# Kernel optimization log

Hardware: AMD Instinct MI355X
Metric: run time of the kernel (lower is better)

Reference implementation:

```python
import jax, jax.numpy as jnp
import numpy as np

MB, NUM, LENTH, SIZE, OUT = 16, 128, 64, 256, 256
DIN = (LENTH + 1) * 2  # aux_lenth = 0


def setup_inputs() -> dict:
    key = jax.random.key(0)
    ks = jax.random.split(key, 9)
    s = 0.05
    return {
        "in_": jax.random.normal(ks[0], (MB, NUM, LENTH), dtype=jnp.float32),
        "W1": jax.random.normal(ks[1], (DIN, SIZE), dtype=jnp.float32) * s,
        "b1": jax.random.normal(ks[2], (SIZE,), dtype=jnp.float32) * s,
        "W2": jax.random.normal(ks[3], (SIZE, SIZE), dtype=jnp.float32) * s,
        "b2": jax.random.normal(ks[4], (SIZE,), dtype=jnp.float32) * s,
        "W3": jax.random.normal(ks[5], (SIZE, SIZE), dtype=jnp.float32) * s,
        "b3": jax.random.normal(ks[6], (SIZE,), dtype=jnp.float32) * s,
        "W4": jax.random.normal(ks[7], (SIZE, OUT), dtype=jnp.float32) * s,
        "b4": jax.random.normal(ks[8], (OUT,), dtype=jnp.float32) * s,
    }


def reference(in_, W1, b1, W2, b2, W3, b3, W4, b4):
    mb, num, _ = in_.shape
    # append coordinate channel: coord[i] = i  -> [mb, num, lenth+1]
    coord = jnp.broadcast_to(
        jnp.arange(num, dtype=in_.dtype)[None, :, None], (mb, num, 1)
    )
    x = jnp.concatenate([in_, coord], axis=2)  # [mb, num, L1], L1 = lenth+1
    L1 = x.shape[2]
    # pairwise: x_full[b, a, j] = concat(x[b, j], x[b, a])
    x_i = jnp.broadcast_to(x[:, None, :, :], (mb, num, num, L1))  # varies over j
    x_j = jnp.broadcast_to(x[:, :, None, :], (mb, num, num, L1))  # varies over a
    x_full = jnp.concatenate([x_i, x_j], axis=3)  # [mb, num, num, 2*L1]
    h = x_full.reshape(mb * num * num, 2 * L1)
    h = jax.nn.relu(h @ W1 + b1)
    h = jax.nn.relu(h @ W2 + b2)
    h = jax.nn.relu(h @ W3 + b3)
    h = jax.nn.relu(h @ W4 + b4)  # [mb*num*num, OUT]
    x_g = h.reshape(mb, num * num, -1).sum(axis=1)  # [mb, OUT]
    return x_g
```

## Files before the change

kernel.cpp:

```cpp
#include <hip/hip_runtime.h>
#include <hip/hip_bf16.h>

using short8 = __attribute__((ext_vector_type(8))) short;
using f32x4  = __attribute__((ext_vector_type(4))) float;

#define MBATCH 16
#define NUMV   128
#define LEN    64
#define SZ     256

__device__ __forceinline__ unsigned short bfbits(float x) {
  union { float f; unsigned u; } c; c.f = x;
  return (unsigned short)((c.u + 0x8000u) >> 16);
}

__global__ void uv_prep(const float* __restrict__ in_, const float* __restrict__ W1,
                        const float* __restrict__ b1,
                        float* __restrict__ u, float* __restrict__ v) {
  int bn = blockIdx.x;
  int n  = bn & (NUMV - 1);
  int s  = threadIdx.x;
  __shared__ float xs[LEN];
  if (s < LEN) xs[s] = in_[bn * LEN + s];
  __syncthreads();
  float fn = (float)n;
  float uu = fn * W1[64 * SZ + s];
  float vv = fn * W1[129 * SZ + s] + b1[s];
  for (int c = 0; c < LEN; ++c) {
    uu = fmaf(xs[c], W1[c * SZ + s], uu);
    vv = fmaf(xs[c], W1[(65 + c) * SZ + s], vv);
  }
  u[bn * SZ + s] = uu;
  v[bn * SZ + s] = vv;
}

__global__ void w_prep(const float* __restrict__ W2, const float* __restrict__ W3,
                       const float* __restrict__ W4, short* __restrict__ wlay) {
  int L = blockIdx.x >> 3, kb = blockIdx.x & 7;
  const float* W = (L == 0) ? W2 : (L == 1) ? W3 : W4;
  int m = threadIdx.x >> 6, lane = threadIdx.x & 63;
  int l16 = lane & 15, q = lane >> 4;
  for (int wv = 0; wv < 4; ++wv) {
    int ch = wv * 64 + m * 16 + l16;
    short8 pk;
    for (int i = 0; i < 8; ++i)
      pk[i] = (short)bfbits(W[(kb * 32 + q * 8 + i) * SZ + ch]);
    int f = ((L * 8 + kb) * 4 + wv) * 4 + m;
    reinterpret_cast<short8*>(wlay)[f * 64 + lane] = pk;
  }
}

__global__ __launch_bounds__(256, 4) void fused_mlp(
    const float* __restrict__ u, const float* __restrict__ v,
    const short* __restrict__ wlay,
    const float* __restrict__ b2, const float* __restrict__ b3, const float* __restrict__ b4,
    float* __restrict__ partial) {
  __shared__ __align__(16) short hbuf[64 * 256];

  int wg = blockIdx.x;
  int b = wg >> 8, a = (wg >> 1) & 127, jh = wg & 1;
  int tid = threadIdx.x;
  int wave = tid >> 6, lane = tid & 63;
  int l16 = lane & 15, q = lane >> 4;

  const char* wptr = (const char*)wlay + wave * 4096 + lane * 16;

  short8 aw[4];
  #pragma unroll
  for (int m = 0; m < 4; ++m)
    aw[m] = *reinterpret_cast<const short8*>(wptr + m * 1024);

  {
    const float4* ub = (const float4*)(u + (size_t)b * NUMV * SZ) + jh * 64 * 64;
    const float4* vb = (const float4*)(v + ((size_t)b * NUMV + a) * SZ);
    #pragma unroll
    for (int it = 0; it < 16; ++it) {
      int flat = tid + it * 256;
      int jr = flat >> 6, c4 = flat & 63;
      float4 uu = ub[jr * 64 + c4];
      float4 vv = vb[c4];
      unsigned lo = (unsigned)bfbits(fmaxf(uu.x + vv.x, 0.f))
                  | ((unsigned)bfbits(fmaxf(uu.y + vv.y, 0.f)) << 16);
      unsigned hi = (unsigned)bfbits(fmaxf(uu.z + vv.z, 0.f))
                  | ((unsigned)bfbits(fmaxf(uu.w + vv.w, 0.f)) << 16);
      int byte = (jr * 512 + c4 * 8) ^ ((jr & 7) << 4);
      uint2 pk; pk.x = lo; pk.y = hi;
      *reinterpret_cast<uint2*>((char*)hbuf + byte) = pk;
    }
  }

  __syncthreads();

  #pragma unroll
  for (int L = 0; L < 3; ++L) {
    const float* bb = (L == 0) ? b2 : (L == 1) ? b3 : b4;

    f32x4 acc[4][4];
    #pragma unroll
    for (int m = 0; m < 4; ++m)
      #pragma unroll
      for (int n = 0; n < 4; ++n)
        acc[m][n] = f32x4{0.f, 0.f, 0.f, 0.f};

    #pragma unroll
    for (int kb = 0; kb < 8; ++kb) {
      bool more = (L * 8 + kb < 23);
      short8 bfr0, bfr1;
      {
        int row0 = 0 * 16 + l16, row1 = 1 * 16 + l16;
        bfr0 = *reinterpret_cast<const short8*>((char*)hbuf +
               ((row0 * 512 + kb * 64 + q * 16) ^ ((row0 & 7) << 4)));
        bfr1 = *reinterpret_cast<const short8*>((char*)hbuf +
               ((row1 * 512 + kb * 64 + q * 16) ^ ((row1 & 7) << 4)));
      }
      #pragma unroll
      for (int m = 0; m < 4; ++m) {
        acc[m][0] = __builtin_amdgcn_mfma_f32_16x16x32_bf16(aw[m], bfr0, acc[m][0], 0, 0, 0);
        acc[m][1] = __builtin_amdgcn_mfma_f32_16x16x32_bf16(aw[m], bfr1, acc[m][1], 0, 0, 0);
      }
      short8 bfr2, bfr3;
      {
        int row2 = 2 * 16 + l16, row3 = 3 * 16 + l16;
        bfr2 = *reinterpret_cast<const short8*>((char*)hbuf +
               ((row2 * 512 + kb * 64 + q * 16) ^ ((row2 & 7) << 4)));
        bfr3 = *reinterpret_cast<const short8*>((char*)hbuf +
               ((row3 * 512 + kb * 64 + q * 16) ^ ((row3 & 7) << 4)));
      }
      #pragma unroll
      for (int m = 0; m < 4; ++m) {
        acc[m][2] = __builtin_amdgcn_mfma_f32_16x16x32_bf16(aw[m], bfr2, acc[m][2], 0, 0, 0);
        acc[m][3] = __builtin_amdgcn_mfma_f32_16x16x32_bf16(aw[m], bfr3, acc[m][3], 0, 0, 0);
        if (more)
          aw[m] = *reinterpret_cast<const short8*>(wptr + 16384 + m * 1024);
      }
      wptr += 16384;
    }

    __syncthreads();

    if (L < 2) {
      #pragma unroll
      for (int m = 0; m < 4; ++m) {
        f32x4 bv = *reinterpret_cast<const f32x4*>(bb + wave * 64 + m * 16 + q * 4);
        int ch = wave * 64 + m * 16 + q * 4;
        #pragma unroll
        for (int n = 0; n < 4; ++n) {
          int row = n * 16 + l16;
          f32x4 t = acc[m][n];
          unsigned lo = (unsigned)bfbits(fmaxf(t[0] + bv[0], 0.f))
                      | ((unsigned)bfbits(fmaxf(t[1] + bv[1], 0.f)) << 16);
          unsigned hi = (unsigned)bfbits(fmaxf(t[2] + bv[2], 0.f))
                      | ((unsigned)bfbits(fmaxf(t[3] + bv[3], 0.f)) << 16);
          int byte = (row * 512 + ch * 2) ^ ((row & 7) << 4);
          uint2 pk; pk.x = lo; pk.y = hi;
          *reinterpret_cast<uint2*>((char*)hbuf + byte) = pk;
        }
      }
      __syncthreads();
    } else {
      #pragma unroll
      for (int m = 0; m < 4; ++m) {
        f32x4 bv = *reinterpret_cast<const f32x4*>(bb + wave * 64 + m * 16 + q * 4);
        f32x4 s = f32x4{0.f, 0.f, 0.f, 0.f};
        #pragma unroll
        for (int n = 0; n < 4; ++n) {
          s[0] += fmaxf(acc[m][n][0] + bv[0], 0.f);
          s[1] += fmaxf(acc[m][n][1] + bv[1], 0.f);
          s[2] += fmaxf(acc[m][n][2] + bv[2], 0.f);
          s[3] += fmaxf(acc[m][n][3] + bv[3], 0.f);
        }
        #pragma unroll
        for (int r = 0; r < 4; ++r) {
          float x = s[r];
          x += __shfl_xor(x, 1);
          x += __shfl_xor(x, 2);
          x += __shfl_xor(x, 4);
          x += __shfl_xor(x, 8);
          s[r] = x;
        }
        if (l16 == 0) {
          float4 o; o.x = s[0]; o.y = s[1]; o.z = s[2]; o.w = s[3];
          *reinterpret_cast<float4*>(partial + (size_t)wg * SZ + wave * 64 + m * 16 + q * 4) = o;
        }
      }
    }
  }
}

__global__ void reduce_partials(const float* __restrict__ partial, float* __restrict__ out) {
  int b = blockIdx.x;
  int s = threadIdx.x;
  const float* p = partial + (size_t)b * 256 * SZ + s;
  float acc = 0.f;
  for (int i = 0; i < 256; ++i) acc += p[(size_t)i * SZ];
  out[b * SZ + s] = acc;
}

extern "C" void kernel_launch(void* const* d_in, const int* in_sizes, int n_in,
                              void* d_out, int out_size, void* d_ws, size_t ws_size,
                              hipStream_t stream) {
  const float* in_ = (const float*)d_in[0];
  const float* W1  = (const float*)d_in[1];
  const float* b1  = (const float*)d_in[2];
  const float* W2  = (const float*)d_in[3];
  const float* b2  = (const float*)d_in[4];
  const float* W3  = (const float*)d_in[5];
  const float* b3  = (const float*)d_in[6];
  const float* W4  = (const float*)d_in[7];
  const float* b4  = (const float*)d_in[8];
  float* out = (float*)d_out;

  char* ws = (char*)d_ws;
  float* u       = (float*)(ws);
  float* v       = (float*)(ws + (2u << 20));
  short* wlay    = (short*)(ws + (4u << 20));
  float* partial = (float*)(ws + (4u << 20) + (1u << 19));

  uv_prep<<<MBATCH * NUMV, 256, 0, stream>>>(in_, W1, b1, u, v);
  w_prep<<<24, 256, 0, stream>>>(W2, W3, W4, wlay);
  fused_mlp<<<MBATCH * NUMV * 2, 256, 0, stream>>>(u, v, wlay, b2, b3, b4, partial);
  reduce_partials<<<MBATCH, 256, 0, stream>>>(partial, out);
}
```

Baseline: 150.2 us.

## Split fused MLP rows across eight waves per workgroup

```diff
diff --git a/kernel.cpp b/kernel.cpp
--- a/kernel.cpp
+++ b/kernel.cpp
@@ -50,7 +50,7 @@
   }
 }
 
-__global__ __launch_bounds__(256, 4) void fused_mlp(
+__global__ __launch_bounds__(512, 4) void fused_mlp(
     const float* __restrict__ u, const float* __restrict__ v,
     const short* __restrict__ wlay,
     const float* __restrict__ b2, const float* __restrict__ b3, const float* __restrict__ b4,
@@ -61,9 +61,10 @@
   int b = wg >> 8, a = (wg >> 1) & 127, jh = wg & 1;
   int tid = threadIdx.x;
   int wave = tid >> 6, lane = tid & 63;
+  int wch = wave & 3, wrow = wave >> 2;
   int l16 = lane & 15, q = lane >> 4;
 
-  const char* wptr = (const char*)wlay + wave * 4096 + lane * 16;
+  const char* wptr = (const char*)wlay + wch * 4096 + lane * 16;
 
   short8 aw[4];
   #pragma unroll
@@ -74,8 +75,8 @@
     const float4* ub = (const float4*)(u + (size_t)b * NUMV * SZ) + jh * 64 * 64;
     const float4* vb = (const float4*)(v + ((size_t)b * NUMV + a) * SZ);
     #pragma unroll
-    for (int it = 0; it < 16; ++it) {
-      int flat = tid + it * 256;
+    for (int it = 0; it < 8; ++it) {
+      int flat = tid + it * 512;
       int jr = flat >> 6, c4 = flat & 63;
       float4 uu = ub[jr * 64 + c4];
       float4 vv = vb[c4];
@@ -95,11 +96,11 @@
   for (int L = 0; L < 3; ++L) {
     const float* bb = (L == 0) ? b2 : (L == 1) ? b3 : b4;
 
-    f32x4 acc[4][4];
+    f32x4 acc[4][2];
     #pragma unroll
     for (int m = 0; m < 4; ++m)
       #pragma unroll
-      for (int n = 0; n < 4; ++n)
+      for (int n = 0; n < 2; ++n)
         acc[m][n] = f32x4{0.f, 0.f, 0.f, 0.f};
 
     #pragma unroll
@@ -107,29 +108,18 @@
       bool more = (L * 8 + kb < 23);
       short8 bfr0, bfr1;
       {
-        int row0 = 0 * 16 + l16, row1 = 1 * 16 + l16;
+        int row0 = wrow * 32 + l16, row1 = wrow * 32 + 16 + l16;
         bfr0 = *reinterpret_cast<const short8*>((char*)hbuf +
                ((row0 * 512 + kb * 64 + q * 16) ^ ((row0 & 7) << 4)));
         bfr1 = *reinterpret_cast<const short8*>((char*)hbuf +
                ((row1 * 512 + kb * 64 + q * 16) ^ ((row1 & 7) << 4)));
       }
       #pragma unroll
+      for (int m = 0; m < 4; ++m)
+        acc[m][0] = __builtin_amdgcn_mfma_f32_16x16x32_bf16(aw[m], bfr0, acc[m][0], 0, 0, 0);
+      #pragma unroll
       for (int m = 0; m < 4; ++m) {
-        acc[m][0] = __builtin_amdgcn_mfma_f32_16x16x32_bf16(aw[m], bfr0, acc[m][0], 0, 0, 0);
         acc[m][1] = __builtin_amdgcn_mfma_f32_16x16x32_bf16(aw[m], bfr1, acc[m][1], 0, 0, 0);
-      }
-      short8 bfr2, bfr3;
-      {
-        int row2 = 2 * 16 + l16, row3 = 3 * 16 + l16;
-        bfr2 = *reinterpret_cast<const short8*>((char*)hbuf +
-               ((row2 * 512 + kb * 64 + q * 16) ^ ((row2 & 7) << 4)));
-        bfr3 = *reinterpret_cast<const short8*>((char*)hbuf +
-               ((row3 * 512 + kb * 64 + q * 16) ^ ((row3 & 7) << 4)));
-      }
-      #pragma unroll
-      for (int m = 0; m < 4; ++m) {
-        acc[m][2] = __builtin_amdgcn_mfma_f32_16x16x32_bf16(aw[m], bfr2, acc[m][2], 0, 0, 0);
-        acc[m][3] = __builtin_amdgcn_mfma_f32_16x16x32_bf16(aw[m], bfr3, acc[m][3], 0, 0, 0);
         if (more)
           aw[m] = *reinterpret_cast<const short8*>(wptr + 16384 + m * 1024);
       }
@@ -141,11 +131,11 @@
     if (L < 2) {
       #pragma unroll
       for (int m = 0; m < 4; ++m) {
-        f32x4 bv = *reinterpret_cast<const f32x4*>(bb + wave * 64 + m * 16 + q * 4);
-        int ch = wave * 64 + m * 16 + q * 4;
+        f32x4 bv = *reinterpret_cast<const f32x4*>(bb + wch * 64 + m * 16 + q * 4);
+        int ch = wch * 64 + m * 16 + q * 4;
         #pragma unroll
-        for (int n = 0; n < 4; ++n) {
-          int row = n * 16 + l16;
+        for (int n = 0; n < 2; ++n) {
+          int row = wrow * 32 + n * 16 + l16;
           f32x4 t = acc[m][n];
           unsigned lo = (unsigned)bfbits(fmaxf(t[0] + bv[0], 0.f))
                       | ((unsigned)bfbits(fmaxf(t[1] + bv[1], 0.f)) << 16);
@@ -158,12 +148,13 @@
       }
       __syncthreads();
     } else {
+      float* pbuf = (float*)hbuf;
       #pragma unroll
       for (int m = 0; m < 4; ++m) {
-        f32x4 bv = *reinterpret_cast<const f32x4*>(bb + wave * 64 + m * 16 + q * 4);
+        f32x4 bv = *reinterpret_cast<const f32x4*>(bb + wch * 64 + m * 16 + q * 4);
         f32x4 s = f32x4{0.f, 0.f, 0.f, 0.f};
         #pragma unroll
-        for (int n = 0; n < 4; ++n) {
+        for (int n = 0; n < 2; ++n) {
           s[0] += fmaxf(acc[m][n][0] + bv[0], 0.f);
           s[1] += fmaxf(acc[m][n][1] + bv[1], 0.f);
           s[2] += fmaxf(acc[m][n][2] + bv[2], 0.f);
@@ -180,9 +171,12 @@
         }
         if (l16 == 0) {
           float4 o; o.x = s[0]; o.y = s[1]; o.z = s[2]; o.w = s[3];
-          *reinterpret_cast<float4*>(partial + (size_t)wg * SZ + wave * 64 + m * 16 + q * 4) = o;
-        }
-      }
+          *reinterpret_cast<float4*>(pbuf + wrow * 256 + wch * 64 + m * 16 + q * 4) = o;
+        }
+      }
+      __syncthreads();
+      if (tid < 256)
+        partial[(size_t)wg * SZ + tid] = pbuf[tid] + pbuf[256 + tid];
     }
   }
 }
@@ -218,6 +212,6 @@
 
   uv_prep<<<MBATCH * NUMV, 256, 0, stream>>>(in_, W1, b1, u, v);
   w_prep<<<24, 256, 0, stream>>>(W2, W3, W4, wlay);
-  fused_mlp<<<MBATCH * NUMV * 2, 256, 0, stream>>>(u, v, wlay, b2, b3, b4, partial);
+  fused_mlp<<<MBATCH * NUMV * 2, 512, 0, stream>>>(u, v, wlay, b2, b3, b4, partial);
   reduce_partials<<<MBATCH, 256, 0, stream>>>(partial, out);
 }
```

After: 158.4 us. 5.5% more time.
